# Optimization experiments

Hardware: AMD Instinct MI355X
Metric: run time of the kernel (lower is better)

Reference implementation:

```python
import jax, jax.numpy as jnp
import numpy as np
from jax import lax

B, T, D, H, L = 16, 256, 128, 128, 4  # batch, seq, input_size, hidden, num_layers
NUM_CLASSES = 10
EPS = 1e-5


def instancenorm(x):
    # x: [B, T, C]; InstanceNorm1d normalizes over the length dim (T) per (B, C),
    # biased variance, eps=1e-5, no affine.
    m = x.mean(axis=1, keepdims=True)
    v = x.var(axis=1, keepdims=True)
    return (x - m) / jnp.sqrt(v + EPS)


def lstm_stack(x, Wih, Whh, bih, bhh):
    # x: [B, T, I]; Wih/Whh: [L, 4H, I_or_H]; bih/bhh: [L, 4H]. Gate order i,f,g,o.
    batch = x.shape[0]
    hid = Whh.shape[-1]
    out = x
    for l in range(Wih.shape[0]):
        wih, whh, b = Wih[l], Whh[l], bih[l] + bhh[l]
        h0 = jnp.zeros((batch, hid), dtype=x.dtype)
        c0 = jnp.zeros((batch, hid), dtype=x.dtype)
        xs = out.swapaxes(0, 1)  # [T, B, I]

        def step(carry, xt):
            h, c = carry
            g = xt @ wih.T + h @ whh.T + b
            i, f, gg, o = jnp.split(g, 4, axis=-1)
            c_new = jax.nn.sigmoid(f) * c + jax.nn.sigmoid(i) * jnp.tanh(gg)
            h_new = jax.nn.sigmoid(o) * jnp.tanh(c_new)
            return (h_new, c_new), h_new

        _, hs = lax.scan(step, (h0, c0), xs)
        out = hs.swapaxes(0, 1)  # [B, T, H]
    return out


def setup_inputs() -> dict:
    key = jax.random.key(0)
    ks = jax.random.split(key, 16)
    s = 1.0 / np.sqrt(H)
    u = lambda k, shape: jax.random.uniform(k, shape, jnp.float32, -s, s)
    return {
        "x": jax.random.normal(ks[0], (B, T, D), jnp.float32),
        "Wih": u(ks[1], (L, 4 * H, D)),   # input_size == hidden_size so shapes stack
        "Whh": u(ks[2], (L, 4 * H, H)),
        "bih": u(ks[3], (L, 4 * H)),
        "bhh": u(ks[4], (L, 4 * H)),
        "proj_h_w": u(ks[5], (H, H)),
        "proj_h_b": u(ks[6], (H,)),
        "proj_x_w": u(ks[7], (H, D)),
        "proj_x_b": u(ks[8], (H,)),
        "attn_w": u(ks[9], (H,)),
        "fc_w": u(ks[10], (NUM_CLASSES, H)),
        "fc_b": u(ks[11], (NUM_CLASSES,)),
    }


def reference(x, Wih, Whh, bih, bhh, proj_h_w, proj_h_b, proj_x_w, proj_x_b, attn_w, fc_w, fc_b):
    batch, seq_len, input_dim = x.shape
    # normalize(): means/stdev are detached; torch std is unbiased (ddof=1)
    means = lax.stop_gradient(x.mean(axis=(0, 1), keepdims=True))
    stdev = lax.stop_gradient(x.std(axis=(0, 1), ddof=1, keepdims=True) + EPS)
    x = (x - means) / stdev
    x = instancenorm(x)

    lstm_out = lstm_stack(x, Wih, Whh, bih, bhh)   # dropout is identity in eval
    lstm_out = instancenorm(lstm_out)

    ph = lstm_out @ proj_h_w.T + proj_h_b           # [B, T, H]
    px = x @ proj_x_w.T + proj_x_b                  # [B, T, H]
    px = instancenorm(px)

    # additive attention over expanded [B, T, D, H] (values identical across D,
    # matching the original broadcast/expand semantics)
    combined = jnp.tanh(
        jnp.broadcast_to((ph + px)[:, :, None, :], (batch, seq_len, input_dim, ph.shape[-1]))
    )
    logits = jnp.einsum("btdh,h->btd", combined, attn_w)       # [B, T, D]
    alpha = jax.nn.softmax(logits.reshape(batch, -1), axis=1)   # softmax over T*D
    attention_map = alpha.reshape(batch, seq_len, input_dim)

    # classify: context = sum over (T, D) of lstm_out_ex * alpha
    context = jnp.einsum("bth,btd->bh", ph, attention_map)      # [B, H]
    out = context @ fc_w.T + fc_b                               # [B, num_classes]
    return out, attention_map
```

## Files before the change

### kernel.cpp

```cpp
#include <hip/hip_runtime.h>
#include <math.h>
#include <cstddef>

#define B_ 16
#define T_ 256
#define D_ 128
#define H_ 128
#define L_ 4
#define G_ 512
#define NC_ 10
#define EPS_ 1e-5f
#define C_ 16
#define NCHUNK_ (T_ / C_)

#define HROW_ 144
#define HOFF(k) ((k) + (((k) >> 5) << 2))

typedef float f4v __attribute__((ext_vector_type(4)));

#define LOAD_W8(w, base)                                                   \
    asm volatile(                                                          \
        "global_load_dwordx4 %0, %8, off\n\t"                             \
        "global_load_dwordx4 %1, %8, off offset:16\n\t"                   \
        "global_load_dwordx4 %2, %8, off offset:32\n\t"                   \
        "global_load_dwordx4 %3, %8, off offset:48\n\t"                   \
        "global_load_dwordx4 %4, %8, off offset:64\n\t"                   \
        "global_load_dwordx4 %5, %8, off offset:80\n\t"                   \
        "global_load_dwordx4 %6, %8, off offset:96\n\t"                   \
        "global_load_dwordx4 %7, %8, off offset:112\n\t"                  \
        "s_waitcnt vmcnt(0)"                                               \
        : "=&v"(w[0]), "=&v"(w[1]), "=&v"(w[2]), "=&v"(w[3]),              \
          "=&v"(w[4]), "=&v"(w[5]), "=&v"(w[6]), "=&v"(w[7])               \
        : "v"(base)                                                        \
        : "memory")

#define DOT32R(dst_, warr_, hvarr_)                                        \
    {                                                                      \
        float d0_ = 0.f, d1_ = 0.f;                                        \
        _Pragma("unroll")                                                  \
        for (int j_ = 0; j_ < 8; j_++) {                                   \
            d0_ = fmaf(warr_[j_].x, hvarr_[j_].x, d0_);                    \
            d1_ = fmaf(warr_[j_].y, hvarr_[j_].y, d1_);                    \
            d0_ = fmaf(warr_[j_].z, hvarr_[j_].z, d0_);                    \
            d1_ = fmaf(warr_[j_].w, hvarr_[j_].w, d1_);                    \
        }                                                                  \
        dst_ = d0_ + d1_;                                                  \
    }

__device__ __forceinline__ float sigmoid_(float x) {
    x = fminf(fmaxf(x, -30.f), 30.f);
    return 1.f / (1.f + __expf(-x));
}
__device__ __forceinline__ float tanh_(float x) {
    float ax = fminf(fabsf(x), 15.f);
    float e = __expf(2.f * ax);
    float t = 1.f - 2.f / (e + 1.f);
    return copysignf(t, x);
}
__device__ __forceinline__ void wait_ge_(int* p, int v) {
    if (__hip_atomic_load(p, __ATOMIC_RELAXED, __HIP_MEMORY_SCOPE_AGENT) < v) {
        do { __builtin_amdgcn_s_sleep(1); }
        while (__hip_atomic_load(p, __ATOMIC_RELAXED, __HIP_MEMORY_SCOPE_AGENT) < v);
    }
    (void)__hip_atomic_load(p, __ATOMIC_ACQUIRE, __HIP_MEMORY_SCOPE_AGENT);
}

__global__ __launch_bounds__(512) void stats_bd(const float* __restrict__ x,
                                                float* __restrict__ psum,
                                                float* __restrict__ psq) {
    int blk = blockIdx.x;
    int b = blk >> 4, strip = blk & 15;
    int tid = threadIdx.x;
    int d = tid & 127, r = tid >> 7;
    const float* xb = x + (size_t)b * T_ * D_ + (size_t)strip * 16 * D_;
    float s = 0.f, q = 0.f;
    for (int t = r; t < 16; t += 4) {
        float v = xb[t * D_ + d];
        s += v; q += v * v;
    }
    __shared__ float ls[512], lq[512];
    ls[tid] = s; lq[tid] = q;
    __syncthreads();
    if (r == 0) {
        s = ls[d] + ls[d + 128] + ls[d + 256] + ls[d + 384];
        q = lq[d] + lq[d + 128] + lq[d + 256] + lq[d + 384];
        psum[blk * 128 + d] = s;
        psq[blk * 128 + d] = q;
    }
}

__global__ __launch_bounds__(128) void stats_norm(const float* __restrict__ psum,
                                                  const float* __restrict__ psq,
                                                  float* __restrict__ mu_bd,
                                                  float* __restrict__ invn) {
    int d = threadIdx.x;
    float S = 0.f, Q = 0.f;
    float sb[16], qb[16];
    for (int b = 0; b < 16; b++) {
        float s = 0.f, q = 0.f;
        for (int st = 0; st < 16; st++) {
            s += psum[(b * 16 + st) * 128 + d];
            q += psq[(b * 16 + st) * 128 + d];
        }
        sb[b] = s; qb[b] = q; S += s; Q += q;
    }
    float n = (float)(B_ * T_);
    float m = S / n;
    float varu = (Q - n * m * m) / (n - 1.f);
    float sd = sqrtf(fmaxf(varu, 0.f)) + EPS_;
    for (int b = 0; b < 16; b++) {
        float mu = sb[b] * (1.f / T_);
        float varT = qb[b] * (1.f / T_) - mu * mu;
        mu_bd[b * 128 + d] = mu;
        invn[b * 128 + d] = rsqrtf(fmaxf(varT, 0.f) + EPS_ * sd * sd);
    }
}

__global__ __attribute__((amdgpu_waves_per_eu(2, 2))) __launch_bounds__(512)
void scan_pipe6(const float* __restrict__ x,
                const float* __restrict__ Wih, const float* __restrict__ Whh,
                const float* __restrict__ bih, const float* __restrict__ bhh,
                const float* __restrict__ proj_x_w, const float* __restrict__ proj_x_b,
                const float* __restrict__ mu_bd, const float* __restrict__ invn,
                float* __restrict__ h_glob,
                float* __restrict__ ring,
                float* __restrict__ px,
                float* __restrict__ mu_px, float* __restrict__ inv_px,
                float* __restrict__ mu_ln, float* __restrict__ inv_ln,
                int* __restrict__ flag_h,
                int* __restrict__ flag_g) {
    const int wg = blockIdx.x;
    const int tid = threadIdx.x;
    __shared__ __align__(16) float shbuf[16 * HROW_];

    if (wg < 64) {
        const int r = tid >> 2, q = tid & 3;
        const int l = wg >> 4, b = wg & 15;
        f4v w0[8], w1[8], w2[8], w3[8];
        const float* wl = Whh + (size_t)l * G_ * 128;
        LOAD_W8(w0, wl + ((size_t)(0 * 128 + r)) * 128 + q * 32);
        LOAD_W8(w1, wl + ((size_t)(1 * 128 + r)) * 128 + q * 32);
        LOAD_W8(w2, wl + ((size_t)(2 * 128 + r)) * 128 + q * 32);
        LOAD_W8(w3, wl + ((size_t)(3 * 128 + r)) * 128 + q * 32);
        float c = 0.f;
        if (tid < HROW_) shbuf[tid] = 0.f;
        const float* rsl = ring + ((size_t)l * 16 + b) * (4 * C_ * G_);
        float* hob = h_glob + ((size_t)l * 16 + b) * T_ * 128;
        int* fg = flag_g + l * 16 + b;
        int* fh = flag_h + l * 16 + b;
        float hreg[C_];
        __syncthreads();

        for (int k = 0; k < NCHUNK_; k++) {
            if (tid == 0) wait_ge_(fg, k + 1);
            __syncthreads();
#pragma unroll
            for (int half = 0; half < 2; half++) {
                float p0[8], p1[8], p2[8], p3[8];
#pragma unroll
                for (int s8 = 0; s8 < 8; s8++) {
                    int s = half * 8 + s8;
                    const float* gp = rsl + ((size_t)(k & 3) * C_ + s) * G_;
                    p0[s8] = __hip_atomic_load(gp + r, __ATOMIC_RELAXED, __HIP_MEMORY_SCOPE_AGENT);
                    p1[s8] = __hip_atomic_load(gp + 128 + r, __ATOMIC_RELAXED, __HIP_MEMORY_SCOPE_AGENT);
                    p2[s8] = __hip_atomic_load(gp + 256 + r, __ATOMIC_RELAXED, __HIP_MEMORY_SCOPE_AGENT);
                    p3[s8] = __hip_atomic_load(gp + 384 + r, __ATOMIC_RELAXED, __HIP_MEMORY_SCOPE_AGENT);
                }
#pragma unroll
                for (int s8 = 0; s8 < 8; s8++) {
                    int s = half * 8 + s8;
                    int t = k * C_ + s;
                    const f4v* hb4 = (const f4v*)(shbuf + (t & 1) * HROW_ + q * 36);
                    f4v hv[8];
#pragma unroll
                    for (int j = 0; j < 8; j++) hv[j] = hb4[j];
                    float zi, zf, zg, zo;
                    DOT32R(zi, w0, hv);
                    DOT32R(zf, w1, hv);
                    DOT32R(zg, w2, hv);
                    DOT32R(zo, w3, hv);
                    zi += __shfl_xor(zi, 1); zi += __shfl_xor(zi, 2);
                    zf += __shfl_xor(zf, 1); zf += __shfl_xor(zf, 2);
                    zg += __shfl_xor(zg, 1); zg += __shfl_xor(zg, 2);
                    zo += __shfl_xor(zo, 1); zo += __shfl_xor(zo, 2);
                    zi += p0[s8]; zf += p1[s8]; zg += p2[s8]; zo += p3[s8];
                    float ai = sigmoid_(zi), af = sigmoid_(zf);
                    float ag = tanh_(zg),    ao = sigmoid_(zo);
                    c = fmaf(af, c, ai * ag);
                    float hn = ao * tanh_(c);
                    if (q == 0) shbuf[((t + 1) & 1) * HROW_ + HOFF(r)] = hn;
                    hreg[s] = hn;
                    __syncthreads();
                }
            }
            if (q == 0) {
#pragma unroll
                for (int s = 0; s < C_; s++)
                    __hip_atomic_store(hob + (size_t)(k * C_ + s) * 128 + r, hreg[s],
                                       __ATOMIC_RELAXED, __HIP_MEMORY_SCOPE_AGENT);
            }
            __syncthreads();
            if (tid == 0) __hip_atomic_store(fh, k + 1, __ATOMIC_RELEASE, __HIP_MEMORY_SCOPE_AGENT);
        }
    } else if (wg < 128) {
        const int r = tid >> 2, q = tid & 3;
        const int l = (wg - 64) >> 4, b = (wg - 64) & 15;
        f4v w0[8], w1[8], w2[8], w3[8];
        const float* wl = Wih + (size_t)l * G_ * 128;
        LOAD_W8(w0, wl + ((size_t)(0 * 128 + r)) * 128 + q * 32);
        LOAD_W8(w1, wl + ((size_t)(1 * 128 + r)) * 128 + q * 32);
        LOAD_W8(w2, wl + ((size_t)(2 * 128 + r)) * 128 + q * 32);
        LOAD_W8(w3, wl + ((size_t)(3 * 128 + r)) * 128 + q * 32);
        float bs0 = bih[l * G_ + r] + bhh[l * G_ + r];
        float bs1 = bih[l * G_ + 128 + r] + bhh[l * G_ + 128 + r];
        float bs2 = bih[l * G_ + 256 + r] + bhh[l * G_ + 256 + r];
        float bs3 = bih[l * G_ + 384 + r] + bhh[l * G_ + 384 + r];
        const float* hsrc = (l > 0) ? h_glob + ((size_t)(l - 1) * 16 + b) * T_ * 128
                                    : x + (size_t)b * T_ * 128;
        float muk = 0.f, ivk = 1.f;
        if (l == 0) { muk = mu_bd[b * 128 + (tid & 127)]; ivk = invn[b * 128 + (tid & 127)]; }
        float* rout = ring + ((size_t)l * 16 + b) * (4 * C_ * G_);
        int* fhp = (l > 0) ? flag_h + (l - 1) * 16 + b : flag_h;
        int* fhme = flag_h + l * 16 + b;
        int* fgo = flag_g + l * 16 + b;

        for (int k = 0; k < NCHUNK_; k++) {
            if (tid == 0) {
                if (l > 0) wait_ge_(fhp, k + 1);
                if (k >= 4) wait_ge_(fhme, k - 3);
            }
            __syncthreads();
#pragma unroll
            for (int i = 0; i < 4; i++) {
                int idx = i * 512 + tid;
                float v;
                if (l == 0) {
                    v = hsrc[(size_t)k * C_ * 128 + idx];
                    v = (v - muk) * ivk;
                } else {
                    v = __hip_atomic_load(hsrc + (size_t)k * C_ * 128 + idx,
                                          __ATOMIC_RELAXED, __HIP_MEMORY_SCOPE_AGENT);
                }
                shbuf[(idx >> 7) * HROW_ + HOFF(idx & 127)] = v;
            }
            __syncthreads();
#pragma unroll
            for (int s = 0; s < C_; s++) {
                const f4v* hb4 = (const f4v*)(shbuf + s * HROW_ + q * 36);
                f4v hv[8];
#pragma unroll
                for (int j = 0; j < 8; j++) hv[j] = hb4[j];
                float z0, z1, z2, z3;
                DOT32R(z0, w0, hv);
                DOT32R(z1, w1, hv);
                DOT32R(z2, w2, hv);
                DOT32R(z3, w3, hv);
                z0 += __shfl_xor(z0, 1); z0 += __shfl_xor(z0, 2);
                z1 += __shfl_xor(z1, 1); z1 += __shfl_xor(z1, 2);
                z2 += __shfl_xor(z2, 1); z2 += __shfl_xor(z2, 2);
                z3 += __shfl_xor(z3, 1); z3 += __shfl_xor(z3, 2);
                if (q == 0) {
                    float* ro = rout + ((size_t)(k & 3) * C_ + s) * G_;
                    __hip_atomic_store(ro + r, z0 + bs0, __ATOMIC_RELAXED, __HIP_MEMORY_SCOPE_AGENT);
                    __hip_atomic_store(ro + 128 + r, z1 + bs1, __ATOMIC_RELAXED, __HIP_MEMORY_SCOPE_AGENT);
                    __hip_atomic_store(ro + 256 + r, z2 + bs2, __ATOMIC_RELAXED, __HIP_MEMORY_SCOPE_AGENT);
                    __hip_atomic_store(ro + 384 + r, z3 + bs3, __ATOMIC_RELAXED, __HIP_MEMORY_SCOPE_AGENT);
                }
            }
            __syncthreads();
            if (tid == 0) __hip_atomic_store(fgo, k + 1, __ATOMIC_RELEASE, __HIP_MEMORY_SCOPE_AGENT);
        }
    } else if (wg < 144) {
        const int b = wg - 128;
        const int h = tid & 127, tq = tid >> 7;
        f4v w0[8], w1[8], w2[8], w3[8];
        LOAD_W8(w0, proj_x_w + (size_t)h * 128 + 0);
        LOAD_W8(w1, proj_x_w + (size_t)h * 128 + 32);
        LOAD_W8(w2, proj_x_w + (size_t)h * 128 + 64);
        LOAD_W8(w3, proj_x_w + (size_t)h * 128 + 96);
        float bsx = proj_x_b[h];
        float muk = mu_bd[b * 128 + h], ivk = invn[b * 128 + h];
        const float* xb = x + (size_t)b * T_ * 128;
        float* pxb = px + (size_t)b * T_ * 128;
        float sacc = 0.f, qacc = 0.f;

        for (int blk = 0; blk < 16; blk++) {
            int t0 = blk * 16;
            __syncthreads();
#pragma unroll
            for (int j = 0; j < 4; j++) {
                int tt = tq * 4 + j;
                float v = xb[(size_t)(t0 + tt) * 128 + h];
                shbuf[tt * HROW_ + HOFF(h)] = (v - muk) * ivk;
            }
            __syncthreads();
#pragma unroll
            for (int j = 0; j < 4; j++) {
                int tt = tq * 4 + j;
                const float* row = shbuf + tt * HROW_;
                f4v hv[8];
                float p0, p1, p2, p3;
                const f4v* r4 = (const f4v*)(row + 0 * 36);
#pragma unroll
                for (int u = 0; u < 8; u++) hv[u] = r4[u];
                DOT32R(p0, w0, hv);
                r4 = (const f4v*)(row + 1 * 36);
#pragma unroll
                for (int u = 0; u < 8; u++) hv[u] = r4[u];
                DOT32R(p1, w1, hv);
                r4 = (const f4v*)(row + 2 * 36);
#pragma unroll
                for (int u = 0; u < 8; u++) hv[u] = r4[u];
                DOT32R(p2, w2, hv);
                r4 = (const f4v*)(row + 3 * 36);
#pragma unroll
                for (int u = 0; u < 8; u++) hv[u] = r4[u];
                DOT32R(p3, w3, hv);
                float val = (p0 + p1) + (p2 + p3) + bsx;
                pxb[(size_t)(t0 + tt) * 128 + h] = val;
                sacc += val; qacc += val * val;
            }
        }
        __syncthreads();
        shbuf[tq * 128 + h] = sacc;
        shbuf[512 + tq * 128 + h] = qacc;
        __syncthreads();
        if (tq == 0) {
            float s = shbuf[h] + shbuf[128 + h] + shbuf[256 + h] + shbuf[384 + h];
            float qq = shbuf[512 + h] + shbuf[640 + h] + shbuf[768 + h] + shbuf[896 + h];
            float m = s * (1.f / T_);
            float v = qq * (1.f / T_) - m * m;
            mu_px[b * 128 + h] = m;
            inv_px[b * 128 + h] = rsqrtf(fmaxf(v, 0.f) + EPS_);
        }
    } else {
        const int b = wg - 144;
        const int h = tid & 127, st = tid >> 7;
        const float* hsrc = h_glob + ((size_t)3 * 16 + b) * T_ * 128;
        int* f3 = flag_h + 3 * 16 + b;
        float s = 0.f, q = 0.f;
        for (int k = 0; k < NCHUNK_; k++) {
            if (tid == 0) wait_ge_(f3, k + 1);
            __syncthreads();
#pragma unroll
            for (int j = 0; j < 4; j++) {
                int tt = st * 4 + j;
                float v = __hip_atomic_load(hsrc + (size_t)(k * C_ + tt) * 128 + h,
                                            __ATOMIC_RELAXED, __HIP_MEMORY_SCOPE_AGENT);
                s += v; q += v * v;
            }
        }
        shbuf[st * 128 + h] = s;
        shbuf[512 + st * 128 + h] = q;
        __syncthreads();
        if (st == 0) {
            float ss = shbuf[h] + shbuf[128 + h] + shbuf[256 + h] + shbuf[384 + h];
            float qq = shbuf[512 + h] + shbuf[640 + h] + shbuf[768 + h] + shbuf[896 + h];
            float m = ss * (1.f / T_);
            float v = qq * (1.f / T_) - m * m;
            mu_ln[b * 128 + h] = m;
            inv_ln[b * 128 + h] = rsqrtf(fmaxf(v, 0.f) + EPS_);
        }
    }
}

__global__ __launch_bounds__(256) void gemm_score(const float* __restrict__ A,
                                                  const float* __restrict__ mu,
                                                  const float* __restrict__ inv,
                                                  const float* __restrict__ Bw,
                                                  const float* __restrict__ b1,
                                                  const float* __restrict__ px,
                                                  const float* __restrict__ mu_px,
                                                  const float* __restrict__ inv_px,
                                                  const float* __restrict__ attn_w,
                                                  float* __restrict__ ph,
                                                  float* __restrict__ lsc) {
    __shared__ __align__(16) float As[16][64];
    __shared__ __align__(16) float Bs[16][128];
    __shared__ float red[64][17];
    int tid = threadIdx.x;
    int m0 = blockIdx.x * 64;
    int lr = tid >> 2, lc = (tid & 3) << 2;
    int lrB = tid >> 1, lcB = (tid & 1) << 3;
    int tr = tid >> 4, tc = tid & 15;
    int tm = tr << 2, tn = tc << 3;
    float acc[4][8] = {};
    int bidx = (m0 + lr) >> 8;
    const float* Arow = A + (size_t)(m0 + lr) * 128 + lc;
    const float* mup = mu + bidx * 128 + lc;
    const float* ivp = inv + bidx * 128 + lc;
    const float* Brow = Bw + (size_t)lrB * 128 + lcB;
    for (int kb = 0; kb < 128; kb += 16) {
        float4 av = *(const float4*)(Arow + kb);
        float4 m4 = *(const float4*)(mup + kb);
        float4 i4 = *(const float4*)(ivp + kb);
        av.x = (av.x - m4.x) * i4.x; av.y = (av.y - m4.y) * i4.y;
        av.z = (av.z - m4.z) * i4.z; av.w = (av.w - m4.w) * i4.w;
        float4 bv0 = *(const float4*)(Brow + kb);
        float4 bv1 = *(const float4*)(Brow + kb + 4);
        __syncthreads();
        As[lc + 0][lr] = av.x; As[lc + 1][lr] = av.y; As[lc + 2][lr] = av.z; As[lc + 3][lr] = av.w;
        Bs[lcB + 0][lrB] = bv0.x; Bs[lcB + 1][lrB] = bv0.y; Bs[lcB + 2][lrB] = bv0.z; Bs[lcB + 3][lrB] = bv0.w;
        Bs[lcB + 4][lrB] = bv1.x; Bs[lcB + 5][lrB] = bv1.y; Bs[lcB + 6][lrB] = bv1.z; Bs[lcB + 7][lrB] = bv1.w;
        __syncthreads();
#pragma unroll
        for (int k = 0; k < 16; k++) {
            float ar[4], br[8];
#pragma unroll
            for (int i = 0; i < 4; i++) ar[i] = As[k][tm + i];
#pragma unroll
            for (int j = 0; j < 8; j++) br[j] = Bs[k][tn + j];
#pragma unroll
            for (int i = 0; i < 4; i++)
#pragma unroll
                for (int j = 0; j < 8; j++)
                    acc[i][j] = fmaf(ar[i], br[j], acc[i][j]);
        }
    }
    float spart[4];
#pragma unroll
    for (int i = 0; i < 4; i++) {
        int row = m0 + tm + i;
        int bb = row >> 8;
        float sp = 0.f;
#pragma unroll
        for (int j = 0; j < 8; j++) {
            int col = tn + j;
            float val = acc[i][j] + b1[col];
            ph[(size_t)row * 128 + col] = val;
            float inx = (px[(size_t)row * 128 + col] - mu_px[bb * 128 + col]) * inv_px[bb * 128 + col];
            sp = fmaf(tanh_(val + inx), attn_w[col], sp);
        }
        spart[i] = sp;
    }
    __syncthreads();
#pragma unroll
    for (int i = 0; i < 4; i++) red[tm + i][tc] = spart[i];
    __syncthreads();
    if (tid < 64) {
        float s = 0.f;
#pragma unroll
        for (int j = 0; j < 16; j++) s += red[tid][j];
        lsc[m0 + tid] = s;
    }
}

__global__ __launch_bounds__(256) void tail4(const float* __restrict__ lsc,
                                             const float* __restrict__ ph,
                                             const float* __restrict__ fc_w,
                                             const float* __restrict__ fc_b,
                                             float* __restrict__ out,
                                             float* __restrict__ out_att) {
    int b = blockIdx.x >> 2, qt = blockIdx.x & 3;
    int tid = threadIdx.x;
    int h = tid & 127, st = tid >> 7;
    const float* phb = ph + (size_t)b * T_ * H_;
    __shared__ float tmp[256], wsh[256], ls[256];
    float v = lsc[b * 256 + tid];
    tmp[tid] = v; __syncthreads();
    for (int off = 128; off > 0; off >>= 1) { if (tid < off) tmp[tid] = fmaxf(tmp[tid], tmp[tid + off]); __syncthreads(); }
    float mx = tmp[0]; __syncthreads();
    float e = __expf(v - mx);
    tmp[tid] = e; __syncthreads();
    for (int off = 128; off > 0; off >>= 1) { if (tid < off) tmp[tid] += tmp[tid + off]; __syncthreads(); }
    wsh[tid] = e / tmp[0];
    __syncthreads();
    {
        float* ob = out_att + (size_t)b * T_ * D_;
        const float invD = 1.f / (float)D_;
        int base = qt * 64 * 128;
        for (int i = tid; i < 64 * 128; i += 256) ob[base + i] = wsh[(base + i) >> 7] * invD;
    }
    if (qt == 0) {
        float acc = 0.f;
        for (int t = st; t < T_; t += 2) acc = fmaf(phb[t * 128 + h], wsh[t], acc);
        ls[tid] = acc;
        __syncthreads();
        if (tid < 128) ls[tid] = ls[tid] + ls[tid + 128];
        __syncthreads();
        if (tid < NC_) {
            float s = fc_b[tid];
            const float* fw = fc_w + tid * 128;
            for (int k = 0; k < 128; k++) s = fmaf(ls[k], fw[k], s);
            out[b * NC_ + tid] = s;
        }
    }
}

extern "C" void kernel_launch(void* const* d_in, const int* in_sizes, int n_in,
                              void* d_out, int out_size, void* d_ws, size_t ws_size,
                              hipStream_t stream) {
    const float* x        = (const float*)d_in[0];
    const float* Wih      = (const float*)d_in[1];
    const float* Whh      = (const float*)d_in[2];
    const float* bih      = (const float*)d_in[3];
    const float* bhh      = (const float*)d_in[4];
    const float* proj_h_w = (const float*)d_in[5];
    const float* proj_h_b = (const float*)d_in[6];
    const float* proj_x_w = (const float*)d_in[7];
    const float* proj_x_b = (const float*)d_in[8];
    const float* attn_w   = (const float*)d_in[9];
    const float* fc_w     = (const float*)d_in[10];
    const float* fc_b     = (const float*)d_in[11];
    float* out = (float*)d_out;

    float* ws = (float*)d_ws;
    const size_t NTD = (size_t)B_ * T_ * D_;
    float* h_glob = ws;
    float* ring   = h_glob + 4 * NTD;
    float* px     = ring + 4 * NTD;
    float* smalls = px + NTD;
    float* psum   = smalls;
    float* psq    = psum + 32768;
    float* mu_bd  = psq + 32768;
    float* invn   = mu_bd + 2048;
    float* mu_ln  = invn + 2048;
    float* inv_ln = mu_ln + 2048;
    float* mu_px  = inv_ln + 2048;
    float* inv_px = mu_px + 2048;
    float* lsc    = inv_px + 2048;
    int*   flags  = (int*)(lsc + 4096);
    int*   flag_h = flags;
    int*   flag_g = flags + 64;
    float* ph = h_glob;
    const float* h3 = h_glob + 3 * NTD;

    hipMemsetAsync((void*)flags, 0, 128 * sizeof(int), stream);

    stats_bd<<<256, 512, 0, stream>>>(x, psum, psq);
    stats_norm<<<1, 128, 0, stream>>>(psum, psq, mu_bd, invn);

    scan_pipe6<<<160, 512, 0, stream>>>(x, Wih, Whh, bih, bhh,
                                        proj_x_w, proj_x_b, mu_bd, invn,
                                        h_glob, ring, px, mu_px, inv_px,
                                        mu_ln, inv_ln, flag_h, flag_g);

    gemm_score<<<64, 256, 0, stream>>>(h3, mu_ln, inv_ln, proj_h_w, proj_h_b,
                                       px, mu_px, inv_px, attn_w, ph, lsc);

    tail4<<<64, 256, 0, stream>>>(lsc, ph, fc_w, fc_b, out, out + B_ * NC_);
}
```

Baseline: 486.2 us.

## Fold score GEMM and softmax tail into persistent scan kernel via flags

Merges the gemm_score and tail4 kernels into the persistent scan kernel as 64 extra workgroups. These wait on new per-batch flags for the px and layer-norm stats, then compute ph, the attention logits, a softmax with a per-batch counter barrier, and the final outputs. The aim is to remove two kernel launches and their boundaries, so the tail work can start as soon as each batch's data is ready. In exchange it relies on spin-waits that need all 224 workgroups to be co-resident, and it increases the kernel's shared memory use.

```diff
diff --git a/kernel.cpp b/kernel.cpp
--- a/kernel.cpp
+++ b/kernel.cpp
@@ -64,6 +64,12 @@
     }
     (void)__hip_atomic_load(p, __ATOMIC_ACQUIRE, __HIP_MEMORY_SCOPE_AGENT);
 }
+__device__ __forceinline__ void ast_(float* p, float v) {
+    __hip_atomic_store(p, v, __ATOMIC_RELAXED, __HIP_MEMORY_SCOPE_AGENT);
+}
+__device__ __forceinline__ float ald_(const float* p) {
+    return __hip_atomic_load(p, __ATOMIC_RELAXED, __HIP_MEMORY_SCOPE_AGENT);
+}
 
 __global__ __launch_bounds__(512) void stats_bd(const float* __restrict__ x,
                                                 float* __restrict__ psum,
@@ -117,21 +123,33 @@
 }
 
 __global__ __attribute__((amdgpu_waves_per_eu(2, 2))) __launch_bounds__(512)
-void scan_pipe6(const float* __restrict__ x,
-                const float* __restrict__ Wih, const float* __restrict__ Whh,
-                const float* __restrict__ bih, const float* __restrict__ bhh,
-                const float* __restrict__ proj_x_w, const float* __restrict__ proj_x_b,
-                const float* __restrict__ mu_bd, const float* __restrict__ invn,
-                float* __restrict__ h_glob,
-                float* __restrict__ ring,
-                float* __restrict__ px,
-                float* __restrict__ mu_px, float* __restrict__ inv_px,
-                float* __restrict__ mu_ln, float* __restrict__ inv_ln,
-                int* __restrict__ flag_h,
-                int* __restrict__ flag_g) {
+void megascan(const float* __restrict__ x,
+              const float* __restrict__ Wih, const float* __restrict__ Whh,
+              const float* __restrict__ bih, const float* __restrict__ bhh,
+              const float* __restrict__ proj_x_w, const float* __restrict__ proj_x_b,
+              const float* __restrict__ proj_h_w, const float* __restrict__ proj_h_b,
+              const float* __restrict__ attn_w,
+              const float* __restrict__ fc_w, const float* __restrict__ fc_b,
+              const float* __restrict__ mu_bd, const float* __restrict__ invn,
+              float* __restrict__ h_glob,
+              float* __restrict__ ring,
+              float* __restrict__ px,
+              float* __restrict__ mu_px, float* __restrict__ inv_px,
+              float* __restrict__ mu_ln, float* __restrict__ inv_ln,
+              float* __restrict__ lsc,
+              float* __restrict__ out, float* __restrict__ out_att,
+              int* __restrict__ flag_h,
+              int* __restrict__ flag_g,
+              int* __restrict__ flag_px,
+              int* __restrict__ flag_ln,
+              int* __restrict__ cnt) {
     const int wg = blockIdx.x;
     const int tid = threadIdx.x;
     __shared__ __align__(16) float shbuf[16 * HROW_];
+    __shared__ __align__(16) float sAs[64][32];
+    __shared__ __align__(16) float sBs[32][132];
+    __shared__ float sred[64][33];
+    __shared__ float stmp[256], swsh[256], sctx[512];
 
     if (wg < 64) {
         const int r = tid >> 2, q = tid & 3;
@@ -161,10 +179,10 @@
                 for (int s8 = 0; s8 < 8; s8++) {
                     int s = half * 8 + s8;
                     const float* gp = rsl + ((size_t)(k & 3) * C_ + s) * G_;
-                    p0[s8] = __hip_atomic_load(gp + r, __ATOMIC_RELAXED, __HIP_MEMORY_SCOPE_AGENT);
-                    p1[s8] = __hip_atomic_load(gp + 128 + r, __ATOMIC_RELAXED, __HIP_MEMORY_SCOPE_AGENT);
-                    p2[s8] = __hip_atomic_load(gp + 256 + r, __ATOMIC_RELAXED, __HIP_MEMORY_SCOPE_AGENT);
-                    p3[s8] = __hip_atomic_load(gp + 384 + r, __ATOMIC_RELAXED, __HIP_MEMORY_SCOPE_AGENT);
+                    p0[s8] = ald_(gp + r);
+                    p1[s8] = ald_(gp + 128 + r);
+                    p2[s8] = ald_(gp + 256 + r);
+                    p3[s8] = ald_(gp + 384 + r);
                 }
 #pragma unroll
                 for (int s8 = 0; s8 < 8; s8++) {
@@ -196,8 +214,7 @@
             if (q == 0) {
 #pragma unroll
                 for (int s = 0; s < C_; s++)
-                    __hip_atomic_store(hob + (size_t)(k * C_ + s) * 128 + r, hreg[s],
-                                       __ATOMIC_RELAXED, __HIP_MEMORY_SCOPE_AGENT);
+                    ast_(hob + (size_t)(k * C_ + s) * 128 + r, hreg[s]);
             }
             __syncthreads();
             if (tid == 0) __hip_atomic_store(fh, k + 1, __ATOMIC_RELEASE, __HIP_MEMORY_SCOPE_AGENT);
@@ -238,8 +255,7 @@
                     v = hsrc[(size_t)k * C_ * 128 + idx];
                     v = (v - muk) * ivk;
                 } else {
-                    v = __hip_atomic_load(hsrc + (size_t)k * C_ * 128 + idx,
-                                          __ATOMIC_RELAXED, __HIP_MEMORY_SCOPE_AGENT);
+                    v = ald_(hsrc + (size_t)k * C_ * 128 + idx);
                 }
                 shbuf[(idx >> 7) * HROW_ + HOFF(idx & 127)] = v;
             }
@@ -261,10 +277,10 @@
                 z3 += __shfl_xor(z3, 1); z3 += __shfl_xor(z3, 2);
                 if (q == 0) {
                     float* ro = rout + ((size_t)(k & 3) * C_ + s) * G_;
-                    __hip_atomic_store(ro + r, z0 + bs0, __ATOMIC_RELAXED, __HIP_MEMORY_SCOPE_AGENT);
-                    __hip_atomic_store(ro + 128 + r, z1 + bs1, __ATOMIC_RELAXED, __HIP_MEMORY_SCOPE_AGENT);
-                    __hip_atomic_store(ro + 256 + r, z2 + bs2, __ATOMIC_RELAXED, __HIP_MEMORY_SCOPE_AGENT);
-                    __hip_atomic_store(ro + 384 + r, z3 + bs3, __ATOMIC_RELAXED, __HIP_MEMORY_SCOPE_AGENT);
+                    ast_(ro + r, z0 + bs0);
+                    ast_(ro + 128 + r, z1 + bs1);
+                    ast_(ro + 256 + r, z2 + bs2);
+                    ast_(ro + 384 + r, z3 + bs3);
                 }
             }
             __syncthreads();
@@ -317,7 +333,7 @@
                 for (int u = 0; u < 8; u++) hv[u] = r4[u];
                 DOT32R(p3, w3, hv);
                 float val = (p0 + p1) + (p2 + p3) + bsx;
-                pxb[(size_t)(t0 + tt) * 128 + h] = val;
+                ast_(pxb + (size_t)(t0 + tt) * 128 + h, val);
                 sacc += val; qacc += val * val;
             }
         }
@@ -330,10 +346,12 @@
             float qq = shbuf[512 + h] + shbuf[640 + h] + shbuf[768 + h] + shbuf[896 + h];
             float m = s * (1.f / T_);
             float v = qq * (1.f / T_) - m * m;
-            mu_px[b * 128 + h] = m;
-            inv_px[b * 128 + h] = rsqrtf(fmaxf(v, 0.f) + EPS_);
-        }
-    } else {
+            ast_(mu_px + b * 128 + h, m);
+            ast_(inv_px + b * 128 + h, rsqrtf(fmaxf(v, 0.f) + EPS_));
+        }
+        __syncthreads();
+        if (tid == 0) __hip_atomic_store(flag_px + b, 1, __ATOMIC_RELEASE, __HIP_MEMORY_SCOPE_AGENT);
+    } else if (wg < 160) {
         const int b = wg - 144;
         const int h = tid & 127, st = tid >> 7;
         const float* hsrc = h_glob + ((size_t)3 * 16 + b) * T_ * 128;
@@ -345,8 +363,7 @@
 #pragma unroll
             for (int j = 0; j < 4; j++) {
                 int tt = st * 4 + j;
-                float v = __hip_atomic_load(hsrc + (size_t)(k * C_ + tt) * 128 + h,
-                                            __ATOMIC_RELAXED, __HIP_MEMORY_SCOPE_AGENT);
+                float v = ald_(hsrc + (size_t)(k * C_ + tt) * 128 + h);
                 s += v; q += v * v;
             }
         }
@@ -358,131 +375,133 @@
             float qq = shbuf[512 + h] + shbuf[640 + h] + shbuf[768 + h] + shbuf[896 + h];
             float m = ss * (1.f / T_);
             float v = qq * (1.f / T_) - m * m;
-            mu_ln[b * 128 + h] = m;
-            inv_ln[b * 128 + h] = rsqrtf(fmaxf(v, 0.f) + EPS_);
-        }
-    }
-}
-
-__global__ __launch_bounds__(256) void gemm_score(const float* __restrict__ A,
-                                                  const float* __restrict__ mu,
-                                                  const float* __restrict__ inv,
-                                                  const float* __restrict__ Bw,
-                                                  const float* __restrict__ b1,
-                                                  const float* __restrict__ px,
-                                                  const float* __restrict__ mu_px,
-                                                  const float* __restrict__ inv_px,
-                                                  const float* __restrict__ attn_w,
-                                                  float* __restrict__ ph,
-                                                  float* __restrict__ lsc) {
-    __shared__ __align__(16) float As[16][64];
-    __shared__ __align__(16) float Bs[16][128];
-    __shared__ float red[64][17];
-    int tid = threadIdx.x;
-    int m0 = blockIdx.x * 64;
-    int lr = tid >> 2, lc = (tid & 3) << 2;
-    int lrB = tid >> 1, lcB = (tid & 1) << 3;
-    int tr = tid >> 4, tc = tid & 15;
-    int tm = tr << 2, tn = tc << 3;
-    float acc[4][8] = {};
-    int bidx = (m0 + lr) >> 8;
-    const float* Arow = A + (size_t)(m0 + lr) * 128 + lc;
-    const float* mup = mu + bidx * 128 + lc;
-    const float* ivp = inv + bidx * 128 + lc;
-    const float* Brow = Bw + (size_t)lrB * 128 + lcB;
-    for (int kb = 0; kb < 128; kb += 16) {
-        float4 av = *(const float4*)(Arow + kb);
-        float4 m4 = *(const float4*)(mup + kb);
-        float4 i4 = *(const float4*)(ivp + kb);
-        av.x = (av.x - m4.x) * i4.x; av.y = (av.y - m4.y) * i4.y;
-        av.z = (av.z - m4.z) * i4.z; av.w = (av.w - m4.w) * i4.w;
-        float4 bv0 = *(const float4*)(Brow + kb);
-        float4 bv1 = *(const float4*)(Brow + kb + 4);
-        __syncthreads();
-        As[lc + 0][lr] = av.x; As[lc + 1][lr] = av.y; As[lc + 2][lr] = av.z; As[lc + 3][lr] = av.w;
-        Bs[lcB + 0][lrB] = bv0.x; Bs[lcB + 1][lrB] = bv0.y; Bs[lcB + 2][lrB] = bv0.z; Bs[lcB + 3][lrB] = bv0.w;
-        Bs[lcB + 4][lrB] = bv1.x; Bs[lcB + 5][lrB] = bv1.y; Bs[lcB + 6][lrB] = bv1.z; Bs[lcB + 7][lrB] = bv1.w;
-        __syncthreads();
-#pragma unroll
-        for (int k = 0; k < 16; k++) {
-            float ar[4], br[8];
-#pragma unroll
-            for (int i = 0; i < 4; i++) ar[i] = As[k][tm + i];
-#pragma unroll
-            for (int j = 0; j < 8; j++) br[j] = Bs[k][tn + j];
-#pragma unroll
-            for (int i = 0; i < 4; i++)
-#pragma unroll
-                for (int j = 0; j < 8; j++)
-                    acc[i][j] = fmaf(ar[i], br[j], acc[i][j]);
-        }
-    }
-    float spart[4];
-#pragma unroll
-    for (int i = 0; i < 4; i++) {
-        int row = m0 + tm + i;
-        int bb = row >> 8;
-        float sp = 0.f;
-#pragma unroll
-        for (int j = 0; j < 8; j++) {
-            int col = tn + j;
-            float val = acc[i][j] + b1[col];
-            ph[(size_t)row * 128 + col] = val;
-            float inx = (px[(size_t)row * 128 + col] - mu_px[bb * 128 + col]) * inv_px[bb * 128 + col];
-            sp = fmaf(tanh_(val + inx), attn_w[col], sp);
-        }
-        spart[i] = sp;
-    }
-    __syncthreads();
-#pragma unroll
-    for (int i = 0; i < 4; i++) red[tm + i][tc] = spart[i];
-    __syncthreads();
-    if (tid < 64) {
-        float s = 0.f;
-#pragma unroll
-        for (int j = 0; j < 16; j++) s += red[tid][j];
-        lsc[m0 + tid] = s;
-    }
-}
-
-__global__ __launch_bounds__(256) void tail4(const float* __restrict__ lsc,
-                                             const float* __restrict__ ph,
-                                             const float* __restrict__ fc_w,
-                                             const float* __restrict__ fc_b,
-                                             float* __restrict__ out,
-                                             float* __restrict__ out_att) {
-    int b = blockIdx.x >> 2, qt = blockIdx.x & 3;
-    int tid = threadIdx.x;
-    int h = tid & 127, st = tid >> 7;
-    const float* phb = ph + (size_t)b * T_ * H_;
-    __shared__ float tmp[256], wsh[256], ls[256];
-    float v = lsc[b * 256 + tid];
-    tmp[tid] = v; __syncthreads();
-    for (int off = 128; off > 0; off >>= 1) { if (tid < off) tmp[tid] = fmaxf(tmp[tid], tmp[tid + off]); __syncthreads(); }
-    float mx = tmp[0]; __syncthreads();
-    float e = __expf(v - mx);
-    tmp[tid] = e; __syncthreads();
-    for (int off = 128; off > 0; off >>= 1) { if (tid < off) tmp[tid] += tmp[tid + off]; __syncthreads(); }
-    wsh[tid] = e / tmp[0];
-    __syncthreads();
-    {
-        float* ob = out_att + (size_t)b * T_ * D_;
-        const float invD = 1.f / (float)D_;
-        int base = qt * 64 * 128;
-        for (int i = tid; i < 64 * 128; i += 256) ob[base + i] = wsh[(base + i) >> 7] * invD;
-    }
-    if (qt == 0) {
-        float acc = 0.f;
-        for (int t = st; t < T_; t += 2) acc = fmaf(phb[t * 128 + h], wsh[t], acc);
-        ls[tid] = acc;
-        __syncthreads();
-        if (tid < 128) ls[tid] = ls[tid] + ls[tid + 128];
-        __syncthreads();
-        if (tid < NC_) {
-            float s = fc_b[tid];
-            const float* fw = fc_w + tid * 128;
-            for (int k = 0; k < 128; k++) s = fmaf(ls[k], fw[k], s);
-            out[b * NC_ + tid] = s;
+            ast_(mu_ln + b * 128 + h, m);
+            ast_(inv_ln + b * 128 + h, rsqrtf(fmaxf(v, 0.f) + EPS_));
+        }
+        __syncthreads();
+        if (tid == 0) __hip_atomic_store(flag_ln + b, 1, __ATOMIC_RELEASE, __HIP_MEMORY_SCOPE_AGENT);
+    } else {
+        const int blk = wg - 160;
+        const int b = blk >> 2, qt = blk & 3;
+        const int m0 = qt * 64;
+        if (tid == 0) { wait_ge_(flag_px + b, 1); wait_ge_(flag_ln + b, 1); }
+        __syncthreads();
+
+        const float* h3b = h_glob + ((size_t)3 * 16 + b) * T_ * 128;
+        float* phg = h_glob;
+        const int lr = tid >> 3, lc = (tid & 7) << 2;
+        const int nB = tid >> 2, k0B = (tid & 3) << 3;
+        const int tm = (tid >> 5) << 2, tn = (tid & 31) << 2;
+        float acc[4][4] = {};
+        const float* mup = mu_ln + b * 128;
+        const float* ivp = inv_ln + b * 128;
+        for (int kb = 0; kb < 128; kb += 32) {
+            float4 av = *(const float4*)(h3b + (size_t)(m0 + lr) * 128 + kb + lc);
+            float4 m4 = *(const float4*)(mup + kb + lc);
+            float4 i4 = *(const float4*)(ivp + kb + lc);
+            av.x = (av.x - m4.x) * i4.x; av.y = (av.y - m4.y) * i4.y;
+            av.z = (av.z - m4.z) * i4.z; av.w = (av.w - m4.w) * i4.w;
+            float4 bv0 = *(const float4*)(proj_h_w + (size_t)nB * 128 + kb + k0B);
+            float4 bv1 = *(const float4*)(proj_h_w + (size_t)nB * 128 + kb + k0B + 4);
+            __syncthreads();
+            *(float4*)&sAs[lr][lc] = av;
+            sBs[k0B + 0][nB] = bv0.x; sBs[k0B + 1][nB] = bv0.y;
+            sBs[k0B + 2][nB] = bv0.z; sBs[k0B + 3][nB] = bv0.w;
+            sBs[k0B + 4][nB] = bv1.x; sBs[k0B + 5][nB] = bv1.y;
+            sBs[k0B + 6][nB] = bv1.z; sBs[k0B + 7][nB] = bv1.w;
+            __syncthreads();
+#pragma unroll
+            for (int k4 = 0; k4 < 8; k4++) {
+                f4v a4[4];
+#pragma unroll
+                for (int i = 0; i < 4; i++) a4[i] = *(const f4v*)&sAs[tm + i][k4 * 4];
+#pragma unroll
+                for (int kk = 0; kk < 4; kk++) {
+                    f4v b4 = *(const f4v*)&sBs[k4 * 4 + kk][tn];
+#pragma unroll
+                    for (int i = 0; i < 4; i++) {
+                        acc[i][0] = fmaf(a4[i][kk], b4.x, acc[i][0]);
+                        acc[i][1] = fmaf(a4[i][kk], b4.y, acc[i][1]);
+                        acc[i][2] = fmaf(a4[i][kk], b4.z, acc[i][2]);
+                        acc[i][3] = fmaf(a4[i][kk], b4.w, acc[i][3]);
+                    }
+                }
+            }
+        }
+        float spart[4];
+#pragma unroll
+        for (int i = 0; i < 4; i++) {
+            int t = m0 + tm + i;
+            size_t prow = ((size_t)b * 256 + t) * 128;
+            float sp = 0.f;
+#pragma unroll
+            for (int j = 0; j < 4; j++) {
+                int col = tn + j;
+                float val = acc[i][j] + proj_h_b[col];
+                ast_(phg + prow + col, val);
+                float inx = (ald_(px + prow + col) - ald_(mu_px + b * 128 + col))
+                            * ald_(inv_px + b * 128 + col);
+                sp = fmaf(tanh_(val + inx), attn_w[col], sp);
+            }
+            spart[i] = sp;
+        }
+        __syncthreads();
+#pragma unroll
+        for (int i = 0; i < 4; i++) sred[tm + i][tid & 31] = spart[i];
+        __syncthreads();
+        if (tid < 64) {
+            float s = 0.f;
+#pragma unroll
+            for (int j = 0; j < 32; j++) s += sred[tid][j];
+            ast_(lsc + b * 256 + m0 + tid, s);
+        }
+        __syncthreads();
+        if (tid == 0) {
+            (void)__hip_atomic_fetch_add(cnt + b, 1, __ATOMIC_ACQ_REL, __HIP_MEMORY_SCOPE_AGENT);
+            wait_ge_(cnt + b, 4);
+        }
+        __syncthreads();
+        float v = 0.f;
+        if (tid < 256) { v = ald_(lsc + b * 256 + tid); stmp[tid] = v; }
+        __syncthreads();
+        for (int off = 128; off > 0; off >>= 1) {
+            if (tid < off) stmp[tid] = fmaxf(stmp[tid], stmp[tid + off]);
+            __syncthreads();
+        }
+        float mx = stmp[0];
+        __syncthreads();
+        float e = (tid < 256) ? __expf(v - mx) : 0.f;
+        if (tid < 256) stmp[tid] = e;
+        __syncthreads();
+        for (int off = 128; off > 0; off >>= 1) {
+            if (tid < off) stmp[tid] += stmp[tid + off];
+            __syncthreads();
+        }
+        float tot = stmp[0];
+        __syncthreads();
+        if (tid < 256) swsh[tid] = e / tot;
+        __syncthreads();
+        {
+            float* ob = out_att + (size_t)b * T_ * D_ + (size_t)m0 * 128;
+            const float invD = 1.f / (float)D_;
+            for (int i = tid; i < 64 * 128; i += 512)
+                ob[i] = swsh[m0 + (i >> 7)] * invD;
+        }
+        if (qt == 0) {
+            int h = tid & 127, st = tid >> 7;
+            float a = 0.f;
+            for (int tt = st * 64; tt < st * 64 + 64; tt++)
+                a = fmaf(phg[((size_t)b * 256 + tt) * 128 + h], swsh[tt], a);
+            sctx[st * 128 + h] = a;
+            __syncthreads();
+            if (tid < 128) sctx[tid] = sctx[tid] + sctx[128 + tid] + sctx[256 + tid] + sctx[384 + tid];
+            __syncthreads();
+            if (tid < NC_) {
+                float s = fc_b[tid];
+                const float* fw = fc_w + tid * 128;
+                for (int k = 0; k < 128; k++) s = fmaf(sctx[k], fw[k], s);
+                out[b * NC_ + tid] = s;
+            }
         }
     }
 }
@@ -520,23 +539,22 @@
     float* inv_px = mu_px + 2048;
     float* lsc    = inv_px + 2048;
     int*   flags  = (int*)(lsc + 4096);
-    int*   flag_h = flags;
-    int*   flag_g = flags + 64;
-    float* ph = h_glob;
-    const float* h3 = h_glob + 3 * NTD;
-
-    hipMemsetAsync((void*)flags, 0, 128 * sizeof(int), stream);
+    int*   flag_h  = flags;
+    int*   flag_g  = flags + 64;
+    int*   flag_px = flags + 128;
+    int*   flag_ln = flags + 144;
+    int*   cnt     = flags + 160;
+
+    hipMemsetAsync((void*)flags, 0, 256 * sizeof(int), stream);
 
     stats_bd<<<256, 512, 0, stream>>>(x, psum, psq);
     stats_norm<<<1, 128, 0, stream>>>(psum, psq, mu_bd, invn);
 
-    scan_pipe6<<<160, 512, 0, stream>>>(x, Wih, Whh, bih, bhh,
-                                        proj_x_w, proj_x_b, mu_bd, invn,
-                                        h_glob, ring, px, mu_px, inv_px,
-                                        mu_ln, inv_ln, flag_h, flag_g);
-
-    gemm_score<<<64, 256, 0, stream>>>(h3, mu_ln, inv_ln, proj_h_w, proj_h_b,
-                                       px, mu_px, inv_px, attn_w, ph, lsc);
-
-    tail4<<<64, 256, 0, stream>>>(lsc, ph, fc_w, fc_b, out, out + B_ * NC_);
-}
+    megascan<<<224, 512, 0, stream>>>(x, Wih, Whh, bih, bhh,
+                                      proj_x_w, proj_x_b, proj_h_w, proj_h_b,
+                                      attn_w, fc_w, fc_b,
+                                      mu_bd, invn, h_glob, ring, px,
+                                      mu_px, inv_px, mu_ln, inv_ln,
+                                      lsc, out, out + B_ * NC_,
+                                      flag_h, flag_g, flag_px, flag_ln, cnt);
+}
```

After: 462.7 us. 4.8% less time.
